# Performance work log

Measured on AMD Instinct MI355X. Metric: run time of the kernel, lower is better.

## Reference

```python
import jax, jax.numpy as jnp
import numpy as np

N_NODES = 100000
N_EDGES = 1600000
D = 128
HID = 256  # min(2*D, 256)
D_OUT = 128
BN_EPS = 1e-5


def setup_inputs() -> dict:
    key = jax.random.key(0)
    ks = jax.random.split(key, 16)
    s = 0.05
    inp = {
        "x": jax.random.normal(ks[0], (N_NODES, D), dtype=jnp.float32),
        "edges": jax.random.randint(ks[1], (2, N_EDGES), 0, N_NODES, dtype=jnp.int32),
        # affine_before_rnn: Linear(D, D)
        "W_aff": jax.random.normal(ks[2], (D, D), dtype=jnp.float32) * s,
        "b_aff": jnp.zeros((D,), dtype=jnp.float32),
        # GRUCell(D, D)
        "W_ih": jax.random.normal(ks[3], (3 * D, D), dtype=jnp.float32) * s,
        "b_ih": jnp.zeros((3 * D,), dtype=jnp.float32),
        "W_hh": jax.random.normal(ks[4], (3 * D, D), dtype=jnp.float32) * s,
        "b_hh": jnp.zeros((3 * D,), dtype=jnp.float32),
        # merge_layer: Linear(2*D, D)
        "W_merge": jax.random.normal(ks[5], (D, 2 * D), dtype=jnp.float32) * s,
        "b_merge": jnp.zeros((D,), dtype=jnp.float32),
        # learnable self-connection weight
        "eps": jnp.asarray(1.0, dtype=jnp.float32),
        # backbone: Linear(D, HID) -> relu -> Linear(HID, D_OUT) -> relu -> BatchNorm1d
        "W1": jax.random.normal(ks[6], (HID, D), dtype=jnp.float32) * s,
        "b1": jnp.zeros((HID,), dtype=jnp.float32),
        "W2": jax.random.normal(ks[7], (D_OUT, HID), dtype=jnp.float32) * s,
        "b2": jnp.zeros((D_OUT,), dtype=jnp.float32),
        "gamma": jnp.ones((D_OUT,), dtype=jnp.float32),
        "beta": jnp.zeros((D_OUT,), dtype=jnp.float32),
    }
    return inp


def reference(x, edges, W_aff, b_aff, W_ih, b_ih, W_hh, b_hh,
              W_merge, b_merge, eps, W1, b1, W2, b2, gamma, beta):
    src, dst = edges[0], edges[1]
    n = x.shape[0]

    # ---- aggregation 1: 'sum' -> scatter-sum of neighbor features ----
    agg_sum = jax.ops.segment_sum(x[src], dst, num_segments=n)  # (N, D)

    # ---- aggregation 2: 'rnn-max' -> affine, scatter-max, GRUCell ----
    xi = x @ W_aff.T + b_aff
    agg_max = jax.ops.segment_max(xi[src], dst, num_segments=n)  # (N, D)
    agg_max = jnp.where(jnp.isfinite(agg_max), agg_max, 0.0)  # empty segments -> 0

    # GRUCell: input = aggregated neighbors, hidden = original node features
    gi = agg_max @ W_ih.T + b_ih  # (N, 3D)
    gh = x @ W_hh.T + b_hh        # (N, 3D)
    ir, iz, inn = jnp.split(gi, 3, axis=1)
    hr, hz, hn = jnp.split(gh, 3, axis=1)
    r = jax.nn.sigmoid(ir + hr)
    z = jax.nn.sigmoid(iz + hz)
    ncand = jnp.tanh(inn + r * hn)
    rnn_out = (1.0 - z) * ncand + z * x  # (N, D)

    # ---- merge ('cat') ----
    h = jnp.concatenate([agg_sum, rnn_out], axis=1) @ W_merge.T + b_merge  # (N, D)

    # ---- learnable self-connection ----
    h = h + eps * x

    # ---- backbone: dense -> relu -> dense -> relu -> batchnorm1d (train mode) ----
    h = jax.nn.relu(h @ W1.T + b1)
    h = jax.nn.relu(h @ W2.T + b2)
    mean = jnp.mean(h, axis=0)
    var = jnp.mean(jnp.square(h - mean), axis=0)  # biased batch variance
    out = gamma * (h - mean) * jax.lax.rsqrt(var + BN_EPS) + beta
    return out
```

## Files before the change

### kernel.cpp

```cpp
#include <hip/hip_runtime.h>
#include <hip/hip_bf16.h>
#include <math.h>

using bf16 = __hip_bfloat16;
typedef __attribute__((ext_vector_type(8))) short bf16x8;
typedef __attribute__((ext_vector_type(4))) float f32x4;

__device__ __forceinline__ float b2f(unsigned short u) {
  return __uint_as_float(((unsigned)u) << 16);
}
__device__ __forceinline__ unsigned short f2b(float f) {
  bf16 h = __float2bfloat16(f);
  return *reinterpret_cast<unsigned short*>(&h);
}
__device__ __forceinline__ ushort4 f2b4(float4 v) {
  return make_ushort4(f2b(v.x), f2b(v.y), f2b(v.z), f2b(v.w));
}

__global__ __launch_bounds__(256) void mgemm_k(
    const float* __restrict__ x, unsigned short* __restrict__ xcat,
    const float* __restrict__ W, const float* __restrict__ bias, int N) {
  constexpr int LDA = 72;
  __shared__ unsigned short As[128 * LDA];
  __shared__ unsigned short Ws[128 * LDA];

  const int tid = threadIdx.x;
  const int lane = tid & 63;
  const int wave = tid >> 6;
  const int row0 = blockIdx.x * 128;
  const int rowhalf = (wave & 1) * 64;
  const int colhalf = (wave >> 1) * 64;
  const int l15 = lane & 15;
  const int quad = lane >> 4;

  f32x4 acc[4][4] = {};

  for (int kc = 0; kc < 128; kc += 64) {
#pragma unroll
    for (int i = 0; i < 4; i++) {
      int idx = tid + i * 256;
      int r = idx >> 3;
      int k8 = (idx & 7) * 8;
      int row = row0 + r;
      ushort4 u0 = make_ushort4(0, 0, 0, 0), u1 = u0;
      if (row < N) {
        const float* s = x + (size_t)row * 128 + kc + k8;
        u0 = f2b4(*(const float4*)s);
        u1 = f2b4(*(const float4*)(s + 4));
        *(ushort4*)&xcat[(size_t)row * 256 + kc + k8] = u0;
        *(ushort4*)&xcat[(size_t)row * 256 + kc + k8 + 4] = u1;
      }
      *(ushort4*)&As[r * LDA + k8] = u0;
      *(ushort4*)&As[r * LDA + k8 + 4] = u1;
    }
#pragma unroll
    for (int i = 0; i < 8; i++) {
      int idx = tid + i * 256;
      int r = idx >> 4;
      int k4 = idx & 15;
      float4 v = *(const float4*)(W + (size_t)r * 128 + kc + k4 * 4);
      *(ushort4*)&Ws[r * LDA + k4 * 4] = f2b4(v);
    }
    __syncthreads();
#pragma unroll
    for (int ks = 0; ks < 2; ks++) {
      const int ko = ks * 32 + quad * 8;
      bf16x8 af[4], wf[4];
#pragma unroll
      for (int ri = 0; ri < 4; ri++)
        af[ri] = *(const bf16x8*)&As[(rowhalf + ri * 16 + l15) * LDA + ko];
#pragma unroll
      for (int ci = 0; ci < 4; ci++)
        wf[ci] = *(const bf16x8*)&Ws[(colhalf + ci * 16 + l15) * LDA + ko];
#pragma unroll
      for (int ri = 0; ri < 4; ri++)
#pragma unroll
        for (int ci = 0; ci < 4; ci++)
          acc[ri][ci] = __builtin_amdgcn_mfma_f32_16x16x32_bf16(
              af[ri], wf[ci], acc[ri][ci], 0, 0, 0);
    }
    __syncthreads();
  }
#pragma unroll
  for (int ci = 0; ci < 4; ci++) {
    const int col = colhalf + ci * 16 + l15;
    const float bv = bias[col];
#pragma unroll
    for (int ri = 0; ri < 4; ri++) {
      const int rbase = row0 + rowhalf + ri * 16 + quad * 4;
#pragma unroll
      for (int r = 0; r < 4; r++) {
        int row = rbase + r;
        if (row >= N) continue;
        xcat[(size_t)row * 256 + 128 + col] = f2b(acc[ri][ci][r] + bv);
      }
    }
  }
}

__global__ __launch_bounds__(512, 4) void grubb_k(
    const unsigned short* __restrict__ aggm,
    const unsigned short* __restrict__ xcat,
    const unsigned short* __restrict__ aggs,
    const unsigned short* __restrict__ Wbig,
    const float* __restrict__ bias_big,
    const unsigned short* __restrict__ Wmb, const float* __restrict__ bm,
    const unsigned short* __restrict__ W1b, const float* __restrict__ b1,
    const unsigned short* __restrict__ W2b, const float* __restrict__ b2,
    const float* __restrict__ epsp, unsigned short* __restrict__ hout,
    float* __restrict__ pstats, int N) {
  constexpr int LDA = 264;
  constexpr int LDH = 136;
  __shared__ unsigned short As[64 * LDA];
  __shared__ unsigned short Acat[64 * LDA];
  __shared__ float sbn[128], qbn[128];
  unsigned short* Hd = As;
  unsigned short* Hp = Acat;

  const int tid = threadIdx.x;
  const int lane = tid & 63;
  const int wave = tid >> 6;
  const int l15 = lane & 15;
  const int quad = lane >> 4;
  const int row0 = blockIdx.x * 64;
  if (tid < 128) {
    sbn[tid] = 0.f;
    qbn[tid] = 0.f;
  }
  const float ep = epsp[0];
  const int f = wave * 16 + l15;

  {
    int r = tid >> 3;
    int q = tid & 7;
    int row = row0 + r;
    int k32 = q * 32;
    uint4 u[4] = {};
    uint4 v[2] = {};
    if (row < N) {
      const unsigned short* s = (k32 < 128)
                                    ? aggm + (size_t)row * 128 + k32
                                    : xcat + (size_t)row * 256 + (k32 - 128);
#pragma unroll
      for (int i = 0; i < 4; i++) u[i] = *(const uint4*)(s + i * 8);
      const unsigned short* s2 = aggs + (size_t)row * 128 + q * 16;
      v[0] = *(const uint4*)s2;
      v[1] = *(const uint4*)(s2 + 8);
    }
#pragma unroll
    for (int i = 0; i < 4; i++) *(uint4*)&As[r * LDA + k32 + i * 8] = u[i];
    *(uint4*)&Acat[r * LDA + q * 16] = v[0];
    *(uint4*)&Acat[r * LDA + q * 16 + 8] = v[1];
  }
  __syncthreads();

  {
    const unsigned short* wp[4];
#pragma unroll
    for (int g = 0; g < 4; g++)
      wp[g] = Wbig +
              (size_t)((wave >> 1) * 128 + (g + 4 * (wave & 1)) * 16 + l15) *
                  256 +
              quad * 8;
    f32x4 acc[4][4] = {};
    __builtin_amdgcn_s_setprio(1);
#pragma unroll
    for (int ks = 0; ks < 8; ks++) {
      const int ko = ks * 32 + quad * 8;
      bf16x8 af[4];
#pragma unroll
      for (int ri = 0; ri < 4; ri++)
        af[ri] = *(const bf16x8*)&As[(ri * 16 + l15) * LDA + ko];
#pragma unroll
      for (int g = 0; g < 4; g++) {
        if (g == 2 && ks >= 4) continue;
        if (g == 3 && ks < 4) continue;
        bf16x8 wf = *(const bf16x8*)(wp[g] + ks * 32);
#pragma unroll
        for (int ri = 0; ri < 4; ri++)
          acc[ri][g] = __builtin_amdgcn_mfma_f32_16x16x32_bf16(
              af[ri], wf, acc[ri][g], 0, 0, 0);
      }
    }
    __builtin_amdgcn_s_setprio(0);
    const float br = bias_big[f];
    const float bz = bias_big[128 + f];
    const float bi = bias_big[256 + f];
    const float bh = bias_big[384 + f];
#pragma unroll
    for (int ri = 0; ri < 4; ri++) {
#pragma unroll
      for (int r = 0; r < 4; r++) {
        int rl = ri * 16 + quad * 4 + r;
        float rg = 1.f / (1.f + __expf(-(acc[ri][0][r] + br)));
        float zg = 1.f / (1.f + __expf(-(acc[ri][1][r] + bz)));
        float a = acc[ri][2][r] + bi + rg * (acc[ri][3][r] + bh);
        float t = 1.f - 2.f / (__expf(2.f * fabsf(a)) + 1.f);
        float nc = copysignf(t, a);
        float xv = b2f(As[rl * LDA + 128 + f]);
        Acat[rl * LDA + 128 + f] = f2b((1.f - zg) * nc + zg * xv);
      }
    }
  }
  __syncthreads();

  f32x4 accm[4] = {};
  {
    const unsigned short* wptr = Wmb + (size_t)f * 256 + quad * 8;
    __builtin_amdgcn_s_setprio(1);
#pragma unroll
    for (int ks = 0; ks < 8; ks++) {
      const int ko = ks * 32 + quad * 8;
      bf16x8 w0 = *(const bf16x8*)(wptr + ks * 32);
#pragma unroll
      for (int ri = 0; ri < 4; ri++) {
        bf16x8 af = *(const bf16x8*)&Acat[(ri * 16 + l15) * LDA + ko];
        accm[ri] = __builtin_amdgcn_mfma_f32_16x16x32_bf16(af, w0, accm[ri],
                                                           0, 0, 0);
      }
    }
    __builtin_amdgcn_s_setprio(0);
  }
  __syncthreads();
  {
    float bv = bm[f];
#pragma unroll
    for (int ri = 0; ri < 4; ri++) {
#pragma unroll
      for (int r = 0; r < 4; r++) {
        int rl = ri * 16 + quad * 4 + r;
        float v = accm[ri][r] + bv + ep * b2f(As[rl * LDA + 128 + f]);
        Hp[rl * LDH + f] = f2b(v);
      }
    }
  }
  __syncthreads();

  f32x4 acc3[4] = {};
#pragma unroll
  for (int hh = 0; hh < 2; hh++) {
    f32x4 acc2[4] = {};
    {
      const unsigned short* wptr =
          W1b + (size_t)(hh * 128 + f) * 128 + quad * 8;
      __builtin_amdgcn_s_setprio(1);
#pragma unroll
      for (int ks = 0; ks < 4; ks++) {
        const int ko = ks * 32 + quad * 8;
        bf16x8 w0 = *(const bf16x8*)(wptr + ks * 32);
#pragma unroll
        for (int ri = 0; ri < 4; ri++) {
          bf16x8 af = *(const bf16x8*)&Hp[(ri * 16 + l15) * LDH + ko];
          acc2[ri] = __builtin_amdgcn_mfma_f32_16x16x32_bf16(af, w0, acc2[ri],
                                                             0, 0, 0);
        }
      }
      __builtin_amdgcn_s_setprio(0);
    }
    __syncthreads();
    {
      float bv = b1[hh * 128 + f];
#pragma unroll
      for (int ri = 0; ri < 4; ri++) {
#pragma unroll
        for (int r = 0; r < 4; r++) {
          int rl = ri * 16 + quad * 4 + r;
          Hd[rl * LDH + f] = f2b(fmaxf(acc2[ri][r] + bv, 0.f));
        }
      }
    }
    __syncthreads();
    {
      const unsigned short* wptr =
          W2b + (size_t)f * 256 + hh * 128 + quad * 8;
      __builtin_amdgcn_s_setprio(1);
#pragma unroll
      for (int ks = 0; ks < 4; ks++) {
        const int ko = ks * 32 + quad * 8;
        bf16x8 w0 = *(const bf16x8*)(wptr + ks * 32);
#pragma unroll
        for (int ri = 0; ri < 4; ri++) {
          bf16x8 af = *(const bf16x8*)&Hd[(ri * 16 + l15) * LDH + ko];
          acc3[ri] = __builtin_amdgcn_mfma_f32_16x16x32_bf16(af, w0, acc3[ri],
                                                             0, 0, 0);
        }
      }
      __builtin_amdgcn_s_setprio(0);
    }
  }
  {
    float bv = b2[f];
    float s = 0.f, q = 0.f;
#pragma unroll
    for (int ri = 0; ri < 4; ri++) {
#pragma unroll
      for (int r = 0; r < 4; r++) {
        int rl = ri * 16 + quad * 4 + r;
        int row = row0 + rl;
        if (row >= N) continue;
        float v = fmaxf(acc3[ri][r] + bv, 0.f);
        hout[(size_t)row * 128 + f] = f2b(v);
        s += v;
        q += v * v;
      }
    }
    atomicAdd(&sbn[f], s);
    atomicAdd(&qbn[f], q);
  }
  __syncthreads();
  if (tid < 128) {
    float* p = pstats + (size_t)blockIdx.x * 256;
    p[tid] = sbn[tid];
    p[128 + tid] = qbn[tid];
  }
}

__global__ __launch_bounds__(256) void bnred_k(const float* __restrict__ pstats,
                                               float* __restrict__ stats,
                                               int nb) {
  int t = threadIdx.x;
  float s = 0.f;
  for (int b = blockIdx.x; b < nb; b += gridDim.x)
    s += pstats[(size_t)b * 256 + t];
  atomicAdd(&stats[t], s);
}

__global__ __launch_bounds__(256) void prep_k(
    const float* __restrict__ W_ih, const float* __restrict__ b_ih,
    const float* __restrict__ W_hh, const float* __restrict__ b_hh,
    const float* __restrict__ Wm, const float* __restrict__ W1,
    const float* __restrict__ W2, unsigned short* __restrict__ Wbig,
    unsigned short* __restrict__ Wmb, unsigned short* __restrict__ W1b,
    unsigned short* __restrict__ W2b, float* __restrict__ bias_big,
    float* __restrict__ stats, int* __restrict__ deg, int N) {
  int idx = blockIdx.x * 256 + threadIdx.x;
  if (idx < N) deg[idx] = 0;
  if (idx < 32768) {
    int mp = idx >> 6;
    int k4 = (idx & 63) * 4;
    int w = mp >> 7, ci = (mp >> 4) & 7, l15 = mp & 15;
    int g = ci & 3, fi = ci >> 2;
    int f = w * 32 + fi * 16 + l15;
    const float* src = nullptr;
    int koff = 0;
    if (g <= 1) {
      int m = g * 128 + f;
      if (k4 < 128) { src = W_ih + (size_t)m * 128; koff = k4; }
      else          { src = W_hh + (size_t)m * 128; koff = k4 - 128; }
    } else if (g == 2) {
      if (k4 < 128) { src = W_ih + (size_t)(256 + f) * 128; koff = k4; }
    } else {
      if (k4 >= 128) { src = W_hh + (size_t)(256 + f) * 128; koff = k4 - 128; }
    }
    ushort4 o = make_ushort4(0, 0, 0, 0);
    if (src) o = f2b4(*(const float4*)(src + koff));
    *(ushort4*)&Wbig[(size_t)mp * 256 + k4] = o;
  }
  if (idx < 8192) {
    int m = idx >> 6;
    int k4 = (idx & 63) * 4;
    *(ushort4*)&Wmb[(size_t)m * 256 + k4] =
        f2b4(*(const float4*)(Wm + (size_t)m * 256 + k4));
    *(ushort4*)&W2b[(size_t)m * 256 + k4] =
        f2b4(*(const float4*)(W2 + (size_t)m * 256 + k4));
    int m2 = idx >> 5;
    int k42 = (idx & 31) * 4;
    *(ushort4*)&W1b[(size_t)m2 * 128 + k42] =
        f2b4(*(const float4*)(W1 + (size_t)m2 * 128 + k42));
  }
  if (blockIdx.x == 0) {
    int t = threadIdx.x;
    stats[t] = 0.f;
#pragma unroll
    for (int h = 0; h < 2; h++) {
      int mm = t + h * 256;
      float b;
      if (mm < 256) b = b_ih[mm] + b_hh[mm];
      else if (mm < 384) b = b_ih[mm];
      else b = b_hh[mm - 128];
      bias_big[mm] = b;
    }
  }
}

__global__ __launch_bounds__(256) void hist_k(const int* __restrict__ edges,
                                              int* __restrict__ deg, int E) {
  int e = blockIdx.x * 256 + threadIdx.x;
  if (e < E) atomicAdd(&deg[edges[(size_t)E + e]], 1);
}

__global__ __launch_bounds__(256) void scan1_k(const int* __restrict__ deg,
                                               int* __restrict__ off,
                                               int* __restrict__ bsums, int N) {
  __shared__ int s[256];
  int t = threadIdx.x;
  int i = blockIdx.x * 256 + t;
  int v = (i < N) ? deg[i] : 0;
  s[t] = v;
  __syncthreads();
#pragma unroll
  for (int d = 1; d < 256; d <<= 1) {
    int u = (t >= d) ? s[t - d] : 0;
    __syncthreads();
    s[t] += u;
    __syncthreads();
  }
  if (i < N) off[i] = s[t] - v;
  if (t == 255) bsums[blockIdx.x] = s[255];
}

__global__ __launch_bounds__(512) void scan2_k(int* __restrict__ bsums,
                                               int nb) {
  __shared__ int s[512];
  int t = threadIdx.x;
  int v = (t < nb) ? bsums[t] : 0;
  s[t] = v;
  __syncthreads();
#pragma unroll
  for (int d = 1; d < 512; d <<= 1) {
    int u = (t >= d) ? s[t - d] : 0;
    __syncthreads();
    s[t] += u;
    __syncthreads();
  }
  if (t < nb) bsums[t] = s[t] - v;
}

__global__ __launch_bounds__(256) void scan3_k(int* __restrict__ off,
                                               const int* __restrict__ bsums,
                                               int* __restrict__ binoff,
                                               int* __restrict__ bincur,
                                               int N, int E, int NB) {
  int i = blockIdx.x * 256 + threadIdx.x;
  if (i < N) {
    int o = off[i] + bsums[blockIdx.x];
    off[i] = o;
    if ((i & 511) == 0) {
      binoff[i >> 9] = o;
      bincur[i >> 9] = o;
    }
  }
  if (i == 0) {
    off[N] = E;
    binoff[NB] = E;
  }
}

__global__ __launch_bounds__(256) void edgepart_k(const int* __restrict__ edges,
                                                  int* __restrict__ bincur,
                                                  int* __restrict__ part,
                                                  int E, int NB) {
  __shared__ int cnt[256];
  const int tid = threadIdx.x;
  if (tid < NB) cnt[tid] = 0;
  __syncthreads();
  int sv[16], dv[16];
  const int e0 = blockIdx.x * 4096;
#pragma unroll
  for (int i = 0; i < 16; i++) {
    int e = e0 + i * 256 + tid;
    int s = 0, d = -1;
    if (e < E) {
      s = edges[e];
      d = edges[(size_t)E + e];
    }
    sv[i] = s;
    dv[i] = d;
    if (d >= 0) atomicAdd(&cnt[d >> 9], 1);
  }
  __syncthreads();
  if (tid < NB) {
    int c = cnt[tid];
    int base = c ? atomicAdd(&bincur[tid], c) : 0;
    cnt[tid] = base;
  }
  __syncthreads();
#pragma unroll
  for (int i = 0; i < 16; i++) {
    int d = dv[i];
    if (d < 0) continue;
    int p = atomicAdd(&cnt[d >> 9], 1);
    part[p] = (sv[i] << 9) | (d & 511);
  }
}

__global__ __launch_bounds__(1024) void fill2_k(const int* __restrict__ off,
                                                const int* __restrict__ binoff,
                                                const int* __restrict__ part,
                                                int* __restrict__ bucket,
                                                int N) {
  __shared__ int scur[512];
  const int b = blockIdx.x;
  const int n0 = b << 9;
  const int tid = threadIdx.x;
  if (tid < 512) {
    int node = n0 + tid;
    scur[tid] = (node < N) ? off[node] : 0;
  }
  __syncthreads();
  const int j0 = binoff[b];
  const int j1 = binoff[b + 1];
  for (int j = j0 + tid; j < j1; j += 1024) {
    int p = part[j];
    int pos = atomicAdd(&scur[p & 511], 1);
    bucket[pos] = p >> 9;
  }
}

__global__ __launch_bounds__(256) void gather_k(
    const int* __restrict__ off, const int* __restrict__ bucket,
    const unsigned short* __restrict__ xcat, unsigned short* __restrict__ aggm,
    unsigned short* __restrict__ aggs, int N) {
  int node = blockIdx.x * 4 + (threadIdx.x >> 6);
  if (node >= N) return;
  const int lane = threadIdx.x & 63;
  const int half = lane >> 5;
  const int f = (lane & 31) * 4;
  const int j0 = off[node], jend = off[node + 1];
  float s0 = 0.f, s1 = 0.f, s2 = 0.f, s3 = 0.f;
  float m0 = -INFINITY, m1 = -INFINITY, m2 = -INFINITY, m3 = -INFINITY;
  int jj = j0 + half;
  int p0 = (jj < jend) ? bucket[jj] : 0;
  int p1 = (jj + 2 < jend) ? bucket[jj + 2] : 0;
  for (; jj < jend; jj += 2) {
    int src = p0;
    p0 = p1;
    p1 = (jj + 4 < jend) ? bucket[jj + 4] : 0;
    ushort4 a = *(const ushort4*)(xcat + (size_t)src * 256 + f);
    ushort4 b = *(const ushort4*)(xcat + (size_t)src * 256 + 128 + f);
    s0 += b2f(a.x);
    s1 += b2f(a.y);
    s2 += b2f(a.z);
    s3 += b2f(a.w);
    m0 = fmaxf(m0, b2f(b.x));
    m1 = fmaxf(m1, b2f(b.y));
    m2 = fmaxf(m2, b2f(b.z));
    m3 = fmaxf(m3, b2f(b.w));
  }
  s0 += __shfl_xor(s0, 32);
  s1 += __shfl_xor(s1, 32);
  s2 += __shfl_xor(s2, 32);
  s3 += __shfl_xor(s3, 32);
  m0 = fmaxf(m0, __shfl_xor(m0, 32));
  m1 = fmaxf(m1, __shfl_xor(m1, 32));
  m2 = fmaxf(m2, __shfl_xor(m2, 32));
  m3 = fmaxf(m3, __shfl_xor(m3, 32));
  if (half == 0) {
    bool nz = jend > j0;
    ushort4 mv = nz ? make_ushort4(f2b(m0), f2b(m1), f2b(m2), f2b(m3))
                    : make_ushort4(0, 0, 0, 0);
    *(ushort4*)&aggm[(size_t)node * 128 + f] = mv;
    *(ushort4*)&aggs[(size_t)node * 128 + f] =
        make_ushort4(f2b(s0), f2b(s1), f2b(s2), f2b(s3));
  }
}

__global__ __launch_bounds__(256) void bn_apply_k(
    float* __restrict__ out, const unsigned short* __restrict__ hout,
    const float* __restrict__ stats, const float* __restrict__ gamma,
    const float* __restrict__ beta, float invn, int nd4) {
  int g = blockIdx.x * 256 + threadIdx.x;
  if (g >= nd4) return;
  int d = (g & 31) * 4;
  ushort4 hv = ((const ushort4*)hout)[g];
  float o[4] = {b2f(hv.x), b2f(hv.y), b2f(hv.z), b2f(hv.w)};
#pragma unroll
  for (int i = 0; i < 4; i++) {
    float mean = stats[d + i] * invn;
    float var = fmaxf(stats[128 + d + i] * invn - mean * mean, 0.f);
    float sc = gamma[d + i] * rsqrtf(var + 1e-5f);
    o[i] = (o[i] - mean) * sc + beta[d + i];
  }
  ((float4*)out)[g] = make_float4(o[0], o[1], o[2], o[3]);
}

extern "C" void kernel_launch(void* const* d_in, const int* in_sizes, int n_in,
                              void* d_out, int out_size, void* d_ws,
                              size_t ws_size, hipStream_t stream) {
  (void)n_in;
  (void)out_size;
  (void)ws_size;
  const float* x = (const float*)d_in[0];
  const int* edges = (const int*)d_in[1];
  const float* W_aff = (const float*)d_in[2];
  const float* b_aff = (const float*)d_in[3];
  const float* W_ih = (const float*)d_in[4];
  const float* b_ih = (const float*)d_in[5];
  const float* W_hh = (const float*)d_in[6];
  const float* b_hh = (const float*)d_in[7];
  const float* W_merge = (const float*)d_in[8];
  const float* b_merge = (const float*)d_in[9];
  const float* epsp = (const float*)d_in[10];
  const float* W1 = (const float*)d_in[11];
  const float* b1 = (const float*)d_in[12];
  const float* W2 = (const float*)d_in[13];
  const float* b2 = (const float*)d_in[14];
  const float* gamma = (const float*)d_in[15];
  const float* beta = (const float*)d_in[16];

  const int N = in_sizes[0] / 128;
  const int E = in_sizes[1] / 2;
  const size_t nd = (size_t)N * 128;
  const int NB = (N + 511) >> 9;
  const int gblk = (N + 63) / 64;

  char* base = (char*)d_ws;
  unsigned short* xcat = (unsigned short*)base;
  unsigned short* aggs = (unsigned short*)(base + (size_t)N * 512);
  unsigned short* aggm = (unsigned short*)(base + (size_t)N * 1024);
  unsigned short* Wbig = (unsigned short*)(base + (size_t)N * 1280);
  unsigned short* Wmb = Wbig + 512 * 256;
  unsigned short* W1b = Wmb + 128 * 256;
  unsigned short* W2b = W1b + 256 * 128;
  float* bias_big = (float*)(W2b + 128 * 256);
  float* stats = bias_big + 512;
  int* deg = (int*)(stats + 512);
  int* off = deg + N;
  int* binoff = off + N + 1;
  int* bincur = binoff + NB + 1;
  int* bucket = bincur + NB;
  int* bsums = bucket + E;
  float* pstats = (float*)(bsums + ((N + 255) / 256));
  float* out = (float*)d_out;
  unsigned short* hout = aggs;
  int* part = (int*)d_out;

  const int ny = (N + 127) / 128;
  const int nblk = (N + 255) / 256;
  const int eblk = (E + 255) / 256;
  const int pgrid = nblk > 128 ? nblk : 128;
  dim3 blk(256);

  prep_k<<<pgrid, blk, 0, stream>>>(W_ih, b_ih, W_hh, b_hh, W_merge, W1, W2,
                                    Wbig, Wmb, W1b, W2b, bias_big, stats, deg,
                                    N);
  hist_k<<<eblk, blk, 0, stream>>>(edges, deg, E);
  scan1_k<<<nblk, blk, 0, stream>>>(deg, off, bsums, N);
  scan2_k<<<1, 512, 0, stream>>>(bsums, nblk);
  scan3_k<<<nblk, blk, 0, stream>>>(off, bsums, binoff, bincur, N, E, NB);
  edgepart_k<<<(E + 4095) / 4096, blk, 0, stream>>>(edges, bincur, part, E, NB);
  fill2_k<<<NB, dim3(1024), 0, stream>>>(off, binoff, part, bucket, N);

  mgemm_k<<<ny, blk, 0, stream>>>(x, xcat, W_aff, b_aff, N);
  gather_k<<<(N + 3) / 4, blk, 0, stream>>>(off, bucket, xcat, aggm, aggs, N);
  grubb_k<<<gblk, dim3(512), 0, stream>>>(aggm, xcat, aggs, Wbig, bias_big,
                                          Wmb, b_merge, W1b, b1, W2b, b2,
                                          epsp, hout, pstats, N);
  bnred_k<<<64, blk, 0, stream>>>(pstats, stats, gblk);
  bn_apply_k<<<(int)((nd / 4 + 255) / 256), blk, 0, stream>>>(
      out, hout, stats, gamma, beta, 1.f / (float)N, (int)(nd / 4));
}
```

Before: 547.6 us.

## Fuse neighbor gather aggregation into the GRU/backbone GEMM kernel

The separate gather kernel that computed the per-node neighbor sum and max into global buffers is removed. Each 64-row block of the fused GRU/MLP kernel now performs the CSR gather for its own rows and writes the bf16 results straight into shared memory. This drops a global write and re-read of two N×128 bf16 arrays and one kernel launch. The cost is that the irregular, latency-bound gather now runs inside a heavy 512-thread kernel limited by launch bounds and shared memory, which may hide memory latency worse than the standalone gather did.

```diff
diff --git a/kernel.cpp b/kernel.cpp
--- a/kernel.cpp
+++ b/kernel.cpp
@@ -99,9 +99,8 @@
 }
 
 __global__ __launch_bounds__(512, 4) void grubb_k(
-    const unsigned short* __restrict__ aggm,
+    const int* __restrict__ off, const int* __restrict__ bucket,
     const unsigned short* __restrict__ xcat,
-    const unsigned short* __restrict__ aggs,
     const unsigned short* __restrict__ Wbig,
     const float* __restrict__ bias_big,
     const unsigned short* __restrict__ Wmb, const float* __restrict__ bm,
@@ -134,23 +133,61 @@
     int r = tid >> 3;
     int q = tid & 7;
     int row = row0 + r;
-    int k32 = q * 32;
-    uint4 u[4] = {};
-    uint4 v[2] = {};
+    uint4 u0 = {}, u1 = {};
     if (row < N) {
-      const unsigned short* s = (k32 < 128)
-                                    ? aggm + (size_t)row * 128 + k32
-                                    : xcat + (size_t)row * 256 + (k32 - 128);
-#pragma unroll
-      for (int i = 0; i < 4; i++) u[i] = *(const uint4*)(s + i * 8);
-      const unsigned short* s2 = aggs + (size_t)row * 128 + q * 16;
-      v[0] = *(const uint4*)s2;
-      v[1] = *(const uint4*)(s2 + 8);
-    }
-#pragma unroll
-    for (int i = 0; i < 4; i++) *(uint4*)&As[r * LDA + k32 + i * 8] = u[i];
-    *(uint4*)&Acat[r * LDA + q * 16] = v[0];
-    *(uint4*)&Acat[r * LDA + q * 16 + 8] = v[1];
+      const unsigned short* s = xcat + (size_t)row * 256 + q * 16;
+      u0 = *(const uint4*)s;
+      u1 = *(const uint4*)(s + 8);
+    }
+    *(uint4*)&As[r * LDA + 128 + q * 16] = u0;
+    *(uint4*)&As[r * LDA + 128 + q * 16 + 8] = u1;
+  }
+  {
+    const int half = lane >> 5;
+    const int fcol = (lane & 31) * 4;
+#pragma unroll
+    for (int ni = 0; ni < 8; ni++) {
+      int ln = wave * 8 + ni;
+      int node = row0 + ln;
+      if (node >= N) continue;
+      int j0 = off[node], jend = off[node + 1];
+      float s0 = 0.f, s1 = 0.f, s2 = 0.f, s3 = 0.f;
+      float m0 = -INFINITY, m1 = -INFINITY, m2 = -INFINITY, m3 = -INFINITY;
+      int jj = j0 + half;
+      int p0 = (jj < jend) ? bucket[jj] : 0;
+      int p1 = (jj + 2 < jend) ? bucket[jj + 2] : 0;
+      for (; jj < jend; jj += 2) {
+        int src = p0;
+        p0 = p1;
+        p1 = (jj + 4 < jend) ? bucket[jj + 4] : 0;
+        ushort4 a = *(const ushort4*)(xcat + (size_t)src * 256 + fcol);
+        ushort4 b = *(const ushort4*)(xcat + (size_t)src * 256 + 128 + fcol);
+        s0 += b2f(a.x);
+        s1 += b2f(a.y);
+        s2 += b2f(a.z);
+        s3 += b2f(a.w);
+        m0 = fmaxf(m0, b2f(b.x));
+        m1 = fmaxf(m1, b2f(b.y));
+        m2 = fmaxf(m2, b2f(b.z));
+        m3 = fmaxf(m3, b2f(b.w));
+      }
+      s0 += __shfl_xor(s0, 32);
+      s1 += __shfl_xor(s1, 32);
+      s2 += __shfl_xor(s2, 32);
+      s3 += __shfl_xor(s3, 32);
+      m0 = fmaxf(m0, __shfl_xor(m0, 32));
+      m1 = fmaxf(m1, __shfl_xor(m1, 32));
+      m2 = fmaxf(m2, __shfl_xor(m2, 32));
+      m3 = fmaxf(m3, __shfl_xor(m3, 32));
+      if (half == 0) {
+        bool nz = jend > j0;
+        ushort4 mv = nz ? make_ushort4(f2b(m0), f2b(m1), f2b(m2), f2b(m3))
+                        : make_ushort4(0, 0, 0, 0);
+        *(ushort4*)&As[ln * LDA + fcol] = mv;
+        *(ushort4*)&Acat[ln * LDA + fcol] =
+            make_ushort4(f2b(s0), f2b(s1), f2b(s2), f2b(s3));
+      }
+    }
   }
   __syncthreads();
 
@@ -507,54 +544,6 @@
   }
 }
 
-__global__ __launch_bounds__(256) void gather_k(
-    const int* __restrict__ off, const int* __restrict__ bucket,
-    const unsigned short* __restrict__ xcat, unsigned short* __restrict__ aggm,
-    unsigned short* __restrict__ aggs, int N) {
-  int node = blockIdx.x * 4 + (threadIdx.x >> 6);
-  if (node >= N) return;
-  const int lane = threadIdx.x & 63;
-  const int half = lane >> 5;
-  const int f = (lane & 31) * 4;
-  const int j0 = off[node], jend = off[node + 1];
-  float s0 = 0.f, s1 = 0.f, s2 = 0.f, s3 = 0.f;
-  float m0 = -INFINITY, m1 = -INFINITY, m2 = -INFINITY, m3 = -INFINITY;
-  int jj = j0 + half;
-  int p0 = (jj < jend) ? bucket[jj] : 0;
-  int p1 = (jj + 2 < jend) ? bucket[jj + 2] : 0;
-  for (; jj < jend; jj += 2) {
-    int src = p0;
-    p0 = p1;
-    p1 = (jj + 4 < jend) ? bucket[jj + 4] : 0;
-    ushort4 a = *(const ushort4*)(xcat + (size_t)src * 256 + f);
-    ushort4 b = *(const ushort4*)(xcat + (size_t)src * 256 + 128 + f);
-    s0 += b2f(a.x);
-    s1 += b2f(a.y);
-    s2 += b2f(a.z);
-    s3 += b2f(a.w);
-    m0 = fmaxf(m0, b2f(b.x));
-    m1 = fmaxf(m1, b2f(b.y));
-    m2 = fmaxf(m2, b2f(b.z));
-    m3 = fmaxf(m3, b2f(b.w));
-  }
-  s0 += __shfl_xor(s0, 32);
-  s1 += __shfl_xor(s1, 32);
-  s2 += __shfl_xor(s2, 32);
-  s3 += __shfl_xor(s3, 32);
-  m0 = fmaxf(m0, __shfl_xor(m0, 32));
-  m1 = fmaxf(m1, __shfl_xor(m1, 32));
-  m2 = fmaxf(m2, __shfl_xor(m2, 32));
-  m3 = fmaxf(m3, __shfl_xor(m3, 32));
-  if (half == 0) {
-    bool nz = jend > j0;
-    ushort4 mv = nz ? make_ushort4(f2b(m0), f2b(m1), f2b(m2), f2b(m3))
-                    : make_ushort4(0, 0, 0, 0);
-    *(ushort4*)&aggm[(size_t)node * 128 + f] = mv;
-    *(ushort4*)&aggs[(size_t)node * 128 + f] =
-        make_ushort4(f2b(s0), f2b(s1), f2b(s2), f2b(s3));
-  }
-}
-
 __global__ __launch_bounds__(256) void bn_apply_k(
     float* __restrict__ out, const unsigned short* __restrict__ hout,
     const float* __restrict__ stats, const float* __restrict__ gamma,
@@ -606,9 +595,8 @@
 
   char* base = (char*)d_ws;
   unsigned short* xcat = (unsigned short*)base;
-  unsigned short* aggs = (unsigned short*)(base + (size_t)N * 512);
-  unsigned short* aggm = (unsigned short*)(base + (size_t)N * 1024);
-  unsigned short* Wbig = (unsigned short*)(base + (size_t)N * 1280);
+  unsigned short* hout = (unsigned short*)(base + (size_t)N * 512);
+  unsigned short* Wbig = (unsigned short*)(base + (size_t)N * 768);
   unsigned short* Wmb = Wbig + 512 * 256;
   unsigned short* W1b = Wmb + 128 * 256;
   unsigned short* W2b = W1b + 256 * 128;
@@ -622,7 +610,6 @@
   int* bsums = bucket + E;
   float* pstats = (float*)(bsums + ((N + 255) / 256));
   float* out = (float*)d_out;
-  unsigned short* hout = aggs;
   int* part = (int*)d_out;
 
   const int ny = (N + 127) / 128;
@@ -642,8 +629,7 @@
   fill2_k<<<NB, dim3(1024), 0, stream>>>(off, binoff, part, bucket, N);
 
   mgemm_k<<<ny, blk, 0, stream>>>(x, xcat, W_aff, b_aff, N);
-  gather_k<<<(N + 3) / 4, blk, 0, stream>>>(off, bucket, xcat, aggm, aggs, N);
-  grubb_k<<<gblk, dim3(512), 0, stream>>>(aggm, xcat, aggs, Wbig, bias_big,
+  grubb_k<<<gblk, dim3(512), 0, stream>>>(off, bucket, xcat, Wbig, bias_big,
                                           Wmb, b_merge, W1b, b1, W2b, b2,
                                           epsp, hout, pstats, N);
   bnred_k<<<64, blk, 0, stream>>>(pstats, stats, gblk);
```

Result: slower. 594.1 us (+8.5%).
